# Kernel optimization log

Measured on AMD Instinct MI355X. Metric: run time of the kernel, lower is better.

Reference implementation:

```python
import jax, jax.numpy as jnp
import numpy as np

FWD_W = 1.0
BWD_W = 1.0
EPS = 1e-12  # guard sqrt gradient at exact zero


def setup_inputs() -> dict:
    key = jax.random.key(0)
    k1, k2 = jax.random.split(key)
    pred = jax.random.normal(k1, (4, 8192, 3), dtype=jnp.float32)
    target = jax.random.normal(k2, (4, 8192, 3), dtype=jnp.float32)
    return {"pred": pred, "target": target}


def reference(pred, target):
    # pairwise Euclidean distances (torch.cdist, p=2): (B, N, M)
    sq = (jnp.sum(pred * pred, axis=-1)[:, :, None]
          + jnp.sum(target * target, axis=-1)[:, None, :]
          - 2.0 * jnp.einsum('bnd,bmd->bnm', pred, target))
    dist = jnp.sqrt(jnp.maximum(sq, EPS))
    forward_dist = jnp.min(dist, axis=2)   # (B, N): pred -> nearest target
    backward_dist = jnp.min(dist, axis=1)  # (B, M): target -> nearest pred
    total = FWD_W * jnp.sum(forward_dist, axis=1) + BWD_W * jnp.sum(backward_dist, axis=1)
    return jnp.mean(total)  # reduction='mean'
```

## Files before the change

### kernel.cpp

```cpp
#include <hip/hip_runtime.h>
#include <math.h>

#define BATCH   4
#define NPTS    8192
#define THREADS 256
#define NQTOT   (2 * BATCH * NPTS)
#define CHUNK   1024
#define TSPLIT  2
#define THALF   (NPTS / TSPLIT)
#define NCHUNKS (THALF / CHUNK)

typedef _Float16 h8  __attribute__((ext_vector_type(8)));
typedef float    f16v __attribute__((ext_vector_type(16)));

__global__ __launch_bounds__(THREADS)
void chamfer_transform(const float* __restrict__ pred,
                       const float* __restrict__ target,
                       h8* __restrict__ trans_lo,
                       h8* __restrict__ trans_hi)
{
    const int p   = blockIdx.x * THREADS + threadIdx.x;
    const int arr = p >> 15;
    const int pb  = p & 32767;

    const float* src = (arr ? target : pred) + (size_t)pb * 3;
    const float x = src[0], y = src[1], z = src[2];

    const _Float16 hx = (_Float16)x;  const float lxf = x - (float)hx;
    const _Float16 hy = (_Float16)y;  const float lyf = y - (float)hy;
    const _Float16 hz = (_Float16)z;  const float lzf = z - (float)hz;
    const _Float16 lx = (_Float16)lxf, ly = (_Float16)lyf, lz = (_Float16)lzf;

    const float tx = (float)hx + (float)lx;
    const float ty = (float)hy + (float)ly;
    const float tz = (float)hz + (float)lz;
    const float tt = fmaf(tx, tx, fmaf(ty, ty, tz * tz));
    const _Float16 tth = (_Float16)tt;
    const _Float16 ttl = (_Float16)(tt - (float)tth);

    const _Float16 n2 = (_Float16)(-2.0f);
    h8 lo = { n2 * hx, n2 * hy, n2 * hz, tth,
              n2 * hx, n2 * hy, n2 * hz, ttl };
    h8 hi = { n2 * lx, n2 * ly, n2 * lz, (_Float16)0.0f,
              (_Float16)0.0f, (_Float16)0.0f, (_Float16)0.0f, (_Float16)0.0f };

    trans_lo[p] = lo;
    trans_hi[p] = hi;
}

__global__ __launch_bounds__(THREADS, 4)
void chamfer_min_kernel(const float* __restrict__ pred,
                        const float* __restrict__ target,
                        const h8* __restrict__ trans_lo,
                        const h8* __restrict__ trans_hi,
                        float* __restrict__ partial)
{
    __shared__ uint4 slo[CHUNK];
    __shared__ uint4 shi[CHUNK];

    const int tid  = threadIdx.x;
    const int lane = tid & 63;
    const int wave = tid >> 6;
    const int n    = lane & 31;
    const int hi   = lane >> 5;

    const int bid = blockIdx.x;
    const int ts  = bid & 1;
    const int qg  = (bid >> 1) & 63;
    const int b   = (bid >> 7) & 3;
    const int dir = bid >> 9;

    const int  qtbase = qg * 128 + wave * 32;
    const int  tbase  = ts * THALF;
    const int  darr   = (dir == 0) ? 1 : 0;
    const float* qraw = ((dir == 0) ? pred : target) + (size_t)b * NPTS * 3;

    h8 afrag;
    {
        const float* qp = qraw + (size_t)(qtbase + n) * 3;
        const float x = qp[0], y = qp[1], z = qp[2];
        const _Float16 hx = (_Float16)x; const _Float16 lx = (_Float16)(x - (float)hx);
        const _Float16 hy = (_Float16)y; const _Float16 ly = (_Float16)(y - (float)hy);
        const _Float16 hz = (_Float16)z; const _Float16 lz = (_Float16)(z - (float)hz);
        const _Float16 one  = (_Float16)1.0f;
        const _Float16 zero = (_Float16)0.0f;
        if (hi == 0) afrag = (h8){hx, hy, hz, one, lx, ly, lz, one};
        else         afrag = (h8){hx, hy, hz, zero, zero, zero, zero, zero};
    }

    float mn[16];
    #pragma unroll
    for (int i = 0; i < 16; ++i) mn[i] = 3.0e38f;

    const size_t gbase = (size_t)(darr * 4 + b) * NPTS + tbase;
    const h8* bsrc = hi ? (const h8*)shi : (const h8*)slo;

    for (int c = 0; c < NCHUNKS; ++c) {
        const size_t cb = gbase + (size_t)c * CHUNK;
        #pragma unroll
        for (int r = 0; r < 4; ++r) {
            slo[r * THREADS + tid] = ((const uint4*)trans_lo)[cb + r * THREADS + tid];
            shi[r * THREADS + tid] = ((const uint4*)trans_hi)[cb + r * THREADS + tid];
        }
        __syncthreads();

        #pragma unroll 2
        for (int t = 0; t < CHUNK / 32; ++t) {
            const h8 bfrag = bsrc[t * 32 + n];
            f16v zc = {};
            const f16v d = __builtin_amdgcn_mfma_f32_32x32x16_f16(afrag, bfrag, zc, 0, 0, 0);
            #pragma unroll
            for (int i = 0; i < 16; ++i) mn[i] = fminf(mn[i], d[i]);
        }
        __syncthreads();
    }

    #pragma unroll
    for (int mask = 1; mask <= 16; mask <<= 1) {
        #pragma unroll
        for (int i = 0; i < 16; ++i)
            mn[i] = fminf(mn[i], __shfl_xor(mn[i], mask, 64));
    }

    if (n == 0) {
        float* dst = partial + (size_t)ts * NQTOT
                   + (size_t)(dir * 4 + b) * NPTS + qtbase;
        #pragma unroll
        for (int i = 0; i < 16; ++i) {
            const int row = (i & 3) + 8 * (i >> 2) + 4 * hi;
            dst[row] = mn[i];
        }
    }
}

__global__ __launch_bounds__(THREADS)
void chamfer_reduce1(const float* __restrict__ partial,
                     const float* __restrict__ pred,
                     const float* __restrict__ target,
                     float* __restrict__ bsum)
{
    const int tid = threadIdx.x;
    const int i   = blockIdx.x * THREADS + tid;

    const float m = fminf(partial[i], partial[NQTOT + i]);

    const int dir  = i >> 15;
    const int rest = i & 32767;
    const float* qp = ((dir == 0) ? pred : target) + (size_t)rest * 3;
    const float x = qp[0], y = qp[1], z = qp[2];
    const float qq = fmaf(x, x, fmaf(y, y, z * z));

    float acc = sqrtf(fmaxf(qq + m, 1e-12f));

    #pragma unroll
    for (int off = 32; off > 0; off >>= 1)
        acc += __shfl_down(acc, off, 64);

    __shared__ float wsum[4];
    if ((tid & 63) == 0) wsum[tid >> 6] = acc;
    __syncthreads();
    if (tid == 0) bsum[blockIdx.x] = wsum[0] + wsum[1] + wsum[2] + wsum[3];
}

__global__ __launch_bounds__(THREADS)
void chamfer_reduce2(const float* __restrict__ bsum,
                     float* __restrict__ out)
{
    const int tid = threadIdx.x;
    float v = bsum[tid];
    #pragma unroll
    for (int off = 32; off > 0; off >>= 1)
        v += __shfl_down(v, off, 64);

    __shared__ float wsum[4];
    if ((tid & 63) == 0) wsum[tid >> 6] = v;
    __syncthreads();
    if (tid == 0) out[0] = (wsum[0] + wsum[1] + wsum[2] + wsum[3]) * (1.0f / BATCH);
}

extern "C" void kernel_launch(void* const* d_in, const int* in_sizes, int n_in,
                              void* d_out, int out_size, void* d_ws, size_t ws_size,
                              hipStream_t stream)
{
    const float* pred   = (const float*)d_in[0];
    const float* target = (const float*)d_in[1];
    float* out          = (float*)d_out;

    h8*    trans_lo = (h8*)d_ws;
    h8*    trans_hi = (h8*)((char*)d_ws + (size_t)65536 * 16);
    float* partial  = (float*)((char*)d_ws + (size_t)131072 * 16);
    float* bsum     = partial + 2 * NQTOT;

    chamfer_transform<<<NQTOT / THREADS / 1, THREADS, 0, stream>>>(
        pred, target, trans_lo, trans_hi);

    chamfer_min_kernel<<<2 * BATCH * 64 * TSPLIT, THREADS, 0, stream>>>(
        pred, target, trans_lo, trans_hi, partial);

    chamfer_reduce1<<<NQTOT / THREADS, THREADS, 0, stream>>>(
        partial, pred, target, bsum);

    chamfer_reduce2<<<1, THREADS, 0, stream>>>(bsum, out);
}
```

Baseline: 82.82 us.

## Fuse transform, min search and first reduction into one kernel

Drops the separate transform kernel: each block now reads raw fp32 target points, splits them into fp16 hi/lo MFMA fragments on the fly and writes them to shared memory. The target split is removed, so each block scans all 8192 points and the grid shrinks from 1024 to 512 blocks. The sqrt and per-block sum are done in the epilogue, which removes the partial buffer and the first reduce kernel. Launch count goes from four to two, at the cost of recomputing the transform in every block, exposing more per-chunk ALU work before each barrier, and running half as many blocks.

```diff
diff --git a/kernel.cpp b/kernel.cpp
--- a/kernel.cpp
+++ b/kernel.cpp
@@ -4,59 +4,22 @@
 #define BATCH   4
 #define NPTS    8192
 #define THREADS 256
-#define NQTOT   (2 * BATCH * NPTS)
 #define CHUNK   1024
-#define TSPLIT  2
-#define THALF   (NPTS / TSPLIT)
-#define NCHUNKS (THALF / CHUNK)
+#define NCHUNKS (NPTS / CHUNK)
+#define NBLOCKS (2 * BATCH * (NPTS / 128))
 
-typedef _Float16 h8  __attribute__((ext_vector_type(8)));
+typedef _Float16 h8   __attribute__((ext_vector_type(8)));
 typedef float    f16v __attribute__((ext_vector_type(16)));
 
-__global__ __launch_bounds__(THREADS)
-void chamfer_transform(const float* __restrict__ pred,
-                       const float* __restrict__ target,
-                       h8* __restrict__ trans_lo,
-                       h8* __restrict__ trans_hi)
-{
-    const int p   = blockIdx.x * THREADS + threadIdx.x;
-    const int arr = p >> 15;
-    const int pb  = p & 32767;
-
-    const float* src = (arr ? target : pred) + (size_t)pb * 3;
-    const float x = src[0], y = src[1], z = src[2];
-
-    const _Float16 hx = (_Float16)x;  const float lxf = x - (float)hx;
-    const _Float16 hy = (_Float16)y;  const float lyf = y - (float)hy;
-    const _Float16 hz = (_Float16)z;  const float lzf = z - (float)hz;
-    const _Float16 lx = (_Float16)lxf, ly = (_Float16)lyf, lz = (_Float16)lzf;
-
-    const float tx = (float)hx + (float)lx;
-    const float ty = (float)hy + (float)ly;
-    const float tz = (float)hz + (float)lz;
-    const float tt = fmaf(tx, tx, fmaf(ty, ty, tz * tz));
-    const _Float16 tth = (_Float16)tt;
-    const _Float16 ttl = (_Float16)(tt - (float)tth);
-
-    const _Float16 n2 = (_Float16)(-2.0f);
-    h8 lo = { n2 * hx, n2 * hy, n2 * hz, tth,
-              n2 * hx, n2 * hy, n2 * hz, ttl };
-    h8 hi = { n2 * lx, n2 * ly, n2 * lz, (_Float16)0.0f,
-              (_Float16)0.0f, (_Float16)0.0f, (_Float16)0.0f, (_Float16)0.0f };
-
-    trans_lo[p] = lo;
-    trans_hi[p] = hi;
-}
-
-__global__ __launch_bounds__(THREADS, 4)
-void chamfer_min_kernel(const float* __restrict__ pred,
-                        const float* __restrict__ target,
-                        const h8* __restrict__ trans_lo,
-                        const h8* __restrict__ trans_hi,
-                        float* __restrict__ partial)
+__global__ __launch_bounds__(THREADS, 2)
+void chamfer_fused_kernel(const float* __restrict__ pred,
+                          const float* __restrict__ target,
+                          float* __restrict__ bsum)
 {
     __shared__ uint4 slo[CHUNK];
     __shared__ uint4 shi[CHUNK];
+    __shared__ float sqq[128];
+    __shared__ float wsum[8];
 
     const int tid  = threadIdx.x;
     const int lane = tid & 63;
@@ -65,15 +28,14 @@
     const int hi   = lane >> 5;
 
     const int bid = blockIdx.x;
-    const int ts  = bid & 1;
-    const int qg  = (bid >> 1) & 63;
-    const int b   = (bid >> 7) & 3;
-    const int dir = bid >> 9;
+    const int qg  = bid & 63;
+    const int b   = (bid >> 6) & 3;
+    const int dir = bid >> 8;
 
-    const int  qtbase = qg * 128 + wave * 32;
-    const int  tbase  = ts * THALF;
-    const int  darr   = (dir == 0) ? 1 : 0;
     const float* qraw = ((dir == 0) ? pred : target) + (size_t)b * NPTS * 3;
+    const float* draw = ((dir == 0) ? target : pred) + (size_t)b * NPTS * 3;
+
+    const int qtbase = qg * 128 + wave * 32;
 
     h8 afrag;
     {
@@ -84,33 +46,63 @@
         const _Float16 hz = (_Float16)z; const _Float16 lz = (_Float16)(z - (float)hz);
         const _Float16 one  = (_Float16)1.0f;
         const _Float16 zero = (_Float16)0.0f;
-        if (hi == 0) afrag = (h8){hx, hy, hz, one, lx, ly, lz, one};
-        else         afrag = (h8){hx, hy, hz, zero, zero, zero, zero, zero};
+        if (hi == 0) {
+            afrag = (h8){hx, hy, hz, one, lx, ly, lz, one};
+            sqq[wave * 32 + n] = fmaf(x, x, fmaf(y, y, z * z));
+        } else {
+            afrag = (h8){hx, hy, hz, zero, zero, zero, zero, zero};
+        }
     }
 
     float mn[16];
     #pragma unroll
     for (int i = 0; i < 16; ++i) mn[i] = 3.0e38f;
 
-    const size_t gbase = (size_t)(darr * 4 + b) * NPTS + tbase;
-    const h8* bsrc = hi ? (const h8*)shi : (const h8*)slo;
+    const float4* dra4 = (const float4*)draw;
+    const uint4*  bsrc = hi ? shi : slo;
 
     for (int c = 0; c < NCHUNKS; ++c) {
-        const size_t cb = gbase + (size_t)c * CHUNK;
-        #pragma unroll
-        for (int r = 0; r < 4; ++r) {
-            slo[r * THREADS + tid] = ((const uint4*)trans_lo)[cb + r * THREADS + tid];
-            shi[r * THREADS + tid] = ((const uint4*)trans_hi)[cb + r * THREADS + tid];
+        {
+            const int base4 = c * 768 + 3 * tid;
+            const float4 f0 = dra4[base4 + 0];
+            const float4 f1 = dra4[base4 + 1];
+            const float4 f2 = dra4[base4 + 2];
+            const float px[4] = {f0.x, f0.w, f1.z, f2.y};
+            const float py[4] = {f0.y, f1.x, f1.w, f2.z};
+            const float pz[4] = {f0.z, f1.y, f2.x, f2.w};
+
+            #pragma unroll
+            for (int k = 0; k < 4; ++k) {
+                const float x = px[k], y = py[k], z = pz[k];
+                const _Float16 hx = (_Float16)x; const _Float16 lx = (_Float16)(x - (float)hx);
+                const _Float16 hy = (_Float16)y; const _Float16 ly = (_Float16)(y - (float)hy);
+                const _Float16 hz = (_Float16)z; const _Float16 lz = (_Float16)(z - (float)hz);
+                const float tx = (float)hx + (float)lx;
+                const float ty = (float)hy + (float)ly;
+                const float tz = (float)hz + (float)lz;
+                const float tt = fmaf(tx, tx, fmaf(ty, ty, tz * tz));
+                const _Float16 tth = (_Float16)tt;
+                const _Float16 ttl = (_Float16)(tt - (float)tth);
+                const _Float16 n2 = (_Float16)(-2.0f);
+                const _Float16 zz = (_Float16)0.0f;
+                h8 lo = { n2 * hx, n2 * hy, n2 * hz, tth,
+                          n2 * hx, n2 * hy, n2 * hz, ttl };
+                h8 hh = { n2 * lx, n2 * ly, n2 * lz, zz, zz, zz, zz, zz };
+                const int slot = 4 * tid + k;
+                slo[slot] = *(const uint4*)&lo;
+                shi[slot] = *(const uint4*)&hh;
+            }
         }
         __syncthreads();
 
         #pragma unroll 2
         for (int t = 0; t < CHUNK / 32; ++t) {
-            const h8 bfrag = bsrc[t * 32 + n];
-            f16v zc = {};
+            const h8 bfrag = *(const h8*)&bsrc[t * 32 + n];
+            const f16v zc = {};
             const f16v d = __builtin_amdgcn_mfma_f32_32x32x16_f16(afrag, bfrag, zc, 0, 0, 0);
             #pragma unroll
-            for (int i = 0; i < 16; ++i) mn[i] = fminf(mn[i], d[i]);
+            for (int i = 0; i < 16; ++i)
+                mn[i] = fminf(mn[i], d[i]);
         }
         __syncthreads();
     }
@@ -123,51 +115,29 @@
     }
 
     if (n == 0) {
-        float* dst = partial + (size_t)ts * NQTOT
-                   + (size_t)(dir * 4 + b) * NPTS + qtbase;
+        float s = 0.0f;
         #pragma unroll
         for (int i = 0; i < 16; ++i) {
             const int row = (i & 3) + 8 * (i >> 2) + 4 * hi;
-            dst[row] = mn[i];
+            s += sqrtf(fmaxf(sqq[wave * 32 + row] + mn[i], 1e-12f));
         }
+        wsum[wave * 2 + hi] = s;
+    }
+    __syncthreads();
+    if (tid == 0) {
+        float t = 0.0f;
+        #pragma unroll
+        for (int k = 0; k < 8; ++k) t += wsum[k];
+        bsum[bid] = t;
     }
 }
 
 __global__ __launch_bounds__(THREADS)
-void chamfer_reduce1(const float* __restrict__ partial,
-                     const float* __restrict__ pred,
-                     const float* __restrict__ target,
-                     float* __restrict__ bsum)
+void chamfer_final(const float* __restrict__ bsum,
+                   float* __restrict__ out)
 {
     const int tid = threadIdx.x;
-    const int i   = blockIdx.x * THREADS + tid;
-
-    const float m = fminf(partial[i], partial[NQTOT + i]);
-
-    const int dir  = i >> 15;
-    const int rest = i & 32767;
-    const float* qp = ((dir == 0) ? pred : target) + (size_t)rest * 3;
-    const float x = qp[0], y = qp[1], z = qp[2];
-    const float qq = fmaf(x, x, fmaf(y, y, z * z));
-
-    float acc = sqrtf(fmaxf(qq + m, 1e-12f));
-
-    #pragma unroll
-    for (int off = 32; off > 0; off >>= 1)
-        acc += __shfl_down(acc, off, 64);
-
-    __shared__ float wsum[4];
-    if ((tid & 63) == 0) wsum[tid >> 6] = acc;
-    __syncthreads();
-    if (tid == 0) bsum[blockIdx.x] = wsum[0] + wsum[1] + wsum[2] + wsum[3];
-}
-
-__global__ __launch_bounds__(THREADS)
-void chamfer_reduce2(const float* __restrict__ bsum,
-                     float* __restrict__ out)
-{
-    const int tid = threadIdx.x;
-    float v = bsum[tid];
+    float v = bsum[tid] + bsum[tid + 256];
     #pragma unroll
     for (int off = 32; off > 0; off >>= 1)
         v += __shfl_down(v, off, 64);
@@ -185,20 +155,8 @@
     const float* pred   = (const float*)d_in[0];
     const float* target = (const float*)d_in[1];
     float* out          = (float*)d_out;
+    float* bsum         = (float*)d_ws;
 
-    h8*    trans_lo = (h8*)d_ws;
-    h8*    trans_hi = (h8*)((char*)d_ws + (size_t)65536 * 16);
-    float* partial  = (float*)((char*)d_ws + (size_t)131072 * 16);
-    float* bsum     = partial + 2 * NQTOT;
-
-    chamfer_transform<<<NQTOT / THREADS / 1, THREADS, 0, stream>>>(
-        pred, target, trans_lo, trans_hi);
-
-    chamfer_min_kernel<<<2 * BATCH * 64 * TSPLIT, THREADS, 0, stream>>>(
-        pred, target, trans_lo, trans_hi, partial);
-
-    chamfer_reduce1<<<NQTOT / THREADS, THREADS, 0, stream>>>(
-        partial, pred, target, bsum);
-
-    chamfer_reduce2<<<1, THREADS, 0, stream>>>(bsum, out);
+    chamfer_fused_kernel<<<NBLOCKS, THREADS, 0, stream>>>(pred, target, bsum);
+    chamfer_final<<<1, THREADS, 0, stream>>>(bsum, out);
 }
```

Result: slower. 85.99 us (+3.8%).
